# Kernel tuning notes

Hardware: AMD Instinct MI355X
Metric: run time of the kernel (lower is better)

The kernel has to match this reference:

```python
import jax, jax.numpy as jnp
import numpy as np

B, M, D = 512, 100000, 256
EPS = 1e-8  # torch.cosine_similarity eps
TEMP = 10.0  # softmax temperature from source


def setup_inputs() -> dict:
    key = jax.random.key(0)
    kx, kk, kv = jax.random.split(key, 3)
    x = jax.random.normal(kx, (B, D), dtype=jnp.float32)
    memory_keys = jax.random.normal(kk, (M, D), dtype=jnp.float32) * 0.1
    memory_values = jax.random.normal(kv, (M, D), dtype=jnp.float32) * 0.1
    return {"x": x, "memory_keys": memory_keys, "memory_values": memory_values}


def reference(x, memory_keys, memory_values):
    # cosine similarity between x [B,D] and memory_keys [M,D] -> [B,M]
    dots = jnp.einsum("bd,md->bm", x, memory_keys)
    xn = jnp.linalg.norm(x, axis=-1)          # [B]
    kn = jnp.linalg.norm(memory_keys, axis=-1)  # [M]
    denom = jnp.maximum(xn[:, None] * kn[None, :], EPS)
    sims = dots / denom                         # [B,M]
    attn = jax.nn.softmax(sims * TEMP, axis=-1)  # [B,M]
    retrieved = jnp.einsum("bm,md->bd", attn, memory_values)  # [B,D]
    return retrieved, attn
```

## Files before the change

### kernel.cpp

```cpp
#include <hip/hip_runtime.h>
#include <hip/hip_bf16.h>


#define MCOLS 100000
#define MP    100032
#define DDIM  256
#define CHUNK 1664
#define NTFULL 26
#define NCHUNK 61
#define CHUNK1 832
#define NCHUNK1 121
#define NST2  242
#define NSLOT 61
#define ATTN_OFF 131072
#define WS_RXN  0
#define WS_RKN  512
#define WS_RCPL 100512
#define WS_VT_BYTE   1048576ull
#define WS_PART_BYTE 52264960ull
#define WS_KB_BYTE   84246528ull
#define WS_KB_END    (WS_KB_BYTE + 2ull*(size_t)MCOLS*DDIM)

#define GLL(g, l) __builtin_amdgcn_global_load_lds( \
    (const __attribute__((address_space(1))) void*)(g), \
    (__attribute__((address_space(3))) void*)(l), 16, 0, 0)

typedef short short8 __attribute__((ext_vector_type(8)));
typedef float f32x4  __attribute__((ext_vector_type(4)));

static __device__ __forceinline__ unsigned short f2bfu(float f) {
  union { __hip_bfloat16 h; unsigned short u; } cv;
  cv.h = __float2bfloat16(f);
  return cv.u;
}
static __device__ __forceinline__ unsigned int pk2(float a, float b) {
  return (unsigned int)f2bfu(a) | ((unsigned int)f2bfu(b) << 16);
}
static __device__ __forceinline__ short8 pack8(float4 a, float4 b) {
  short8 r;
  r[0] = (short)f2bfu(a.x); r[1] = (short)f2bfu(a.y);
  r[2] = (short)f2bfu(a.z); r[3] = (short)f2bfu(a.w);
  r[4] = (short)f2bfu(b.x); r[5] = (short)f2bfu(b.y);
  r[6] = (short)f2bfu(b.z); r[7] = (short)f2bfu(b.w);
  return r;
}

__global__ void k0_xn(const float* __restrict__ x, float* __restrict__ ws) {
  const int b = blockIdx.x, t = threadIdx.x;
  const float v = x[b*DDIM + t];
  float s = v*v;
  #pragma unroll
  for (int mk = 1; mk <= 32; mk <<= 1) s += __shfl_xor(s, mk);
  __shared__ float ps[4];
  if ((t & 63) == 0) ps[t >> 6] = s;
  __syncthreads();
  if (t == 0) {
    const float tot = ps[0] + ps[1] + ps[2] + ps[3];
    ws[WS_RXN + b] = 10.0f / fmaxf(sqrtf(tot), 1e-12f);
  }
}

template<bool WRITEKB>
__global__ __launch_bounds__(256) void k0c_kn(const float* __restrict__ K,
                                              float* __restrict__ ws) {
  const int t = threadIdx.x;
  const int mg = blockIdx.x*64 + (t >> 2);
  const int qq = t & 3;
  if (mg >= MCOLS) return;
  const float* kp = K + (size_t)mg*DDIM + 64*qq;
  unsigned int* kb = (unsigned int*)((char*)ws + WS_KB_BYTE);
  float ss = 0.f;
  #pragma unroll
  for (int j = 0; j < 8; ++j) {
    const float4 a = *(const float4*)(kp + 8*j);
    const float4 b = *(const float4*)(kp + 8*j + 4);
    ss += a.x*a.x + a.y*a.y + a.z*a.z + a.w*a.w
        + b.x*b.x + b.y*b.y + b.z*b.z + b.w*b.w;
    if (WRITEKB) {
      uint4 u;
      u.x = pk2(a.x, a.y); u.y = pk2(a.z, a.w);
      u.z = pk2(b.x, b.y); u.w = pk2(b.z, b.w);
      const int slot = (8*qq + j) ^ (mg & 7);
      *(uint4*)(kb + (size_t)mg*128 + slot*4) = u;
    }
  }
  ss += __shfl_xor(ss, 1); ss += __shfl_xor(ss, 2);
  if (qq == 0) ws[WS_RKN + mg] = 1.0f / fmaxf(sqrtf(ss), 1e-12f);
}

__global__ __launch_bounds__(256) void k0b_tr(const float* __restrict__ V,
                                              float* __restrict__ ws) {
  const int t = threadIdx.x;
  const int m0 = blockIdx.x * 64;
  __shared__ float vt_f[64][261];
  #pragma unroll
  for (int i = 0; i < 4; ++i) {
    const int ml = (t >> 4) + 16*i;
    const int mg = m0 + ml;
    #pragma unroll
    for (int j = 0; j < 4; ++j) {
      const int d = 4*(t & 15) + 64*j;
      float4 v = make_float4(0.f, 0.f, 0.f, 0.f);
      if (mg < MCOLS) v = *(const float4*)(V + (size_t)mg*DDIM + d);
      vt_f[ml][d] = v.x; vt_f[ml][d+1] = v.y; vt_f[ml][d+2] = v.z; vt_f[ml][d+3] = v.w;
    }
  }
  __syncthreads();
  unsigned short* vt = (unsigned short*)((char*)ws + WS_VT_BYTE);
  const int tl = t & 15;
  const int s = tl >> 1, hf = tl & 1;
  const int mq = 8*s + 4*hf;
  #pragma unroll
  for (int it = 0; it < 16; ++it) {
    const int d = (t >> 4) + 16*it;
    uint2 u;
    u.x = pk2(vt_f[mq+0][d], vt_f[mq+1][d]);
    u.y = pk2(vt_f[mq+2][d], vt_f[mq+3][d]);
    const int sp = s ^ (d & 7);
    *(uint2*)(vt + (size_t)d*MP + m0 + sp*8 + 4*hf) = u;
  }
}

static __device__ __forceinline__ void load_xf(const float* __restrict__ x,
                                               int brow0, int q, int ln,
                                               short8 xf[2][8]) {
  #pragma unroll
  for (int as = 0; as < 2; ++as) {
    const int row = brow0 + 16*as + ln;
    #pragma unroll
    for (int kk = 0; kk < 8; ++kk) {
      const float* p = x + row*DDIM + 32*kk + 8*q;
      xf[as][kk] = pack8(*(const float4*)p, *(const float4*)(p + 4));
    }
  }
}

static __device__ __forceinline__ void stage_k(const char* __restrict__ kb,
                                               int m0, int w, int l,
                                               unsigned short (*klds)[256]) {
  #pragma unroll
  for (int i = 0; i < 4; ++i) {
    int r = m0 + w*8 + i*2 + (l >> 5);
    r = min(r, MCOLS - 1);
    const char* g = kb + (size_t)r*512 + (l & 31)*16;
    char* dst = (char*)&klds[w*8 + i*2][0];
    GLL(g, dst);
  }
}

static __device__ __forceinline__ void stage_vt(const char* __restrict__ vtb,
                                                int m1, int w, int l,
                                                unsigned short (*vtl)[64]) {
  #pragma unroll
  for (int i = 0; i < 4; ++i) {
    const int d = w*32 + i*8 + (l >> 3);
    const int ms = min(m1 + (l & 7)*8, MP - 8);
    const char* g = vtb + ((size_t)d*MP + ms)*2;
    char* dst = (char*)&vtl[w*32 + i*8][0];
    GLL(g, dst);
  }
}

__global__ __launch_bounds__(512, 4) void k1b_sum(const float* __restrict__ x,
                                                  const float* __restrict__ ws,
                                                  float* __restrict__ out) {
  const int bid = blockIdx.x;
  const int c = bid >> 2, rb = bid & 3;
  const int t = threadIdx.x, w = t >> 6, l = t & 63, q = l >> 4, ln = l & 15;
  const int h = w & 1, rg = w >> 1;
  __shared__ __align__(16) unsigned short klds[2][64][256];
  const char* kb = (const char*)ws + WS_KB_BYTE;

  short8 xf[2][8];
  const int brow0 = rb*128 + 32*rg;
  load_xf(x, brow0, q, ln, xf);
  float rxn[2][4];
  #pragma unroll
  for (int as = 0; as < 2; ++as)
    #pragma unroll
    for (int r = 0; r < 4; ++r)
      rxn[as][r] = ws[WS_RXN + brow0 + 16*as + 4*q + r];
  const float* rknw = ws + WS_RKN;
  float lpr[2][4] = {{0.f,0.f,0.f,0.f},{0.f,0.f,0.f,0.f}};
  const int mbase = c*CHUNK1;
  const int nt = min(13, (MCOLS - mbase + 63) >> 6);
  const int l7 = ln & 7;

  stage_k(kb, mbase, w, l, klds[0]);
  __syncthreads();
  for (int mt = 0; mt < nt; ++mt) {
    const int cur = mt & 1;
    const int m0 = mbase + mt*64;
    stage_k(kb, m0 + 64, w, l, klds[cur ^ 1]);
    const char* kbase = (const char*)&klds[cur][0][0];
    const int row0 = 32*h + ln;
    f32x4 acc[2][2];
    #pragma unroll
    for (int as = 0; as < 2; ++as)
      #pragma unroll
      for (int mm = 0; mm < 2; ++mm) { f32x4 z = {0.f,0.f,0.f,0.f}; acc[as][mm] = z; }
    #pragma unroll
    for (int kk = 0; kk < 8; ++kk) {
      const int sl = ((q + 4*kk) ^ l7) << 4;
      const short8 b0 = *(const short8*)(kbase + row0*512 + sl);
      const short8 b1 = *(const short8*)(kbase + (row0 + 16)*512 + sl);
      acc[0][0] = __builtin_amdgcn_mfma_f32_16x16x32_bf16(xf[0][kk], b0, acc[0][0], 0,0,0);
      acc[0][1] = __builtin_amdgcn_mfma_f32_16x16x32_bf16(xf[0][kk], b1, acc[0][1], 0,0,0);
      acc[1][0] = __builtin_amdgcn_mfma_f32_16x16x32_bf16(xf[1][kk], b0, acc[1][0], 0,0,0);
      acc[1][1] = __builtin_amdgcn_mfma_f32_16x16x32_bf16(xf[1][kk], b1, acc[1][1], 0,0,0);
    }
    const int mr0 = m0 + 32*h + ln, mr1 = mr0 + 16;
    const int kr0 = min(mr0, MCOLS-1), kr1 = min(mr1, MCOLS-1);
    const float rk0 = rknw[kr0], rk1 = rknw[kr1];
    const bool ok0 = mr0 < MCOLS, ok1 = mr1 < MCOLS;
    #pragma unroll
    for (int as = 0; as < 2; ++as)
      #pragma unroll
      for (int r = 0; r < 4; ++r)
        lpr[as][r] += (ok0 ? __expf(acc[as][0][r]*rxn[as][r]*rk0) : 0.f)
                    + (ok1 ? __expf(acc[as][1][r]*rxn[as][r]*rk1) : 0.f);
    __syncthreads();
  }
  #pragma unroll
  for (int as = 0; as < 2; ++as)
    #pragma unroll
    for (int r = 0; r < 4; ++r) {
      float s = lpr[as][r];
      s += __shfl_xor(s, 1); s += __shfl_xor(s, 2);
      s += __shfl_xor(s, 4); s += __shfl_xor(s, 8);
      if (ln == 0)
        out[(size_t)(c*2 + h)*512 + brow0 + 16*as + 4*q + r] = s;
    }
}

__global__ void k2_final(const float* __restrict__ out, float* __restrict__ ws) {
  const int b = blockIdx.x, t = threadIdx.x;
  float v = (t < NST2) ? out[(size_t)t*512 + b] : 0.f;
  #pragma unroll
  for (int mk = 1; mk <= 32; mk <<= 1) v += __shfl_xor(v, mk);
  __shared__ float s2[4];
  if ((t & 63) == 0) s2[t >> 6] = v;
  __syncthreads();
  if (t == 0) ws[WS_RCPL + b] = 1.0f / (s2[0] + s2[1] + s2[2] + s2[3]);
}

__global__ __launch_bounds__(512, 2) void k3a_main(const float* __restrict__ x,
                                                   float* __restrict__ ws,
                                                   float* __restrict__ out) {
  const int bid = blockIdx.x;
  const int c = bid >> 2, rb = bid & 3;
  const int t = threadIdx.x, w = t >> 6, l = t & 63, q = l >> 4, ln = l & 15;
  const int h = w & 1, rg = w >> 1;
  __shared__ __align__(16) unsigned short klds[2][64][256];
  __shared__ __align__(16) unsigned short vtl[2][256][64];
  __shared__ __align__(16) unsigned short plds[128][72];
  const char* kb  = (const char*)ws + WS_KB_BYTE;
  const char* vtb = (const char*)ws + WS_VT_BYTE;
  const int R0 = rb*128;

  short8 xf[2][8];
  const int brow0 = R0 + 32*rg;
  load_xf(x, brow0, q, ln, xf);
  float rxn[2][4], rlq[2][4];
  #pragma unroll
  for (int as = 0; as < 2; ++as)
    #pragma unroll
    for (int r = 0; r < 4; ++r) {
      const int row = brow0 + 16*as + 4*q + r;
      rxn[as][r] = ws[WS_RXN  + row];
      rlq[as][r] = ws[WS_RCPL + row];
    }
  f32x4 apv[2][8];
  #pragma unroll
  for (int bs = 0; bs < 2; ++bs)
    #pragma unroll
    for (int dx = 0; dx < 8; ++dx) { f32x4 z = {0.f,0.f,0.f,0.f}; apv[bs][dx] = z; }
  const int b2 = 32*(w & 3), d2 = 128*(w >> 2);
  const float* rknw = ws + WS_RKN;
  float* attn = out + ATTN_OFF;
  const int mbase = c*CHUNK;
  const int nt = min(NTFULL, (MCOLS - mbase + 63) >> 6);
  const int l7 = ln & 7;

  stage_k(kb, mbase, w, l, klds[0]);
  stage_vt(vtb, mbase, w, l, vtl[0]);
  __syncthreads();

  for (int mt = 0; mt < nt; ++mt) {
    const int cur = mt & 1;
    const int m0 = mbase + mt*64;
    stage_k(kb, m0 + 64, w, l, klds[cur ^ 1]);
    const char* kbase = (const char*)&klds[cur][0][0];
    const int row0 = 32*h + ln;
    f32x4 acc[2][2];
    #pragma unroll
    for (int as = 0; as < 2; ++as)
      #pragma unroll
      for (int mm = 0; mm < 2; ++mm) { f32x4 z = {0.f,0.f,0.f,0.f}; acc[as][mm] = z; }
    #pragma unroll
    for (int kk = 0; kk < 8; ++kk) {
      const int sl = ((q + 4*kk) ^ l7) << 4;
      const short8 b0 = *(const short8*)(kbase + row0*512 + sl);
      const short8 b1 = *(const short8*)(kbase + (row0 + 16)*512 + sl);
      acc[0][0] = __builtin_amdgcn_mfma_f32_16x16x32_bf16(xf[0][kk], b0, acc[0][0], 0,0,0);
      acc[0][1] = __builtin_amdgcn_mfma_f32_16x16x32_bf16(xf[0][kk], b1, acc[0][1], 0,0,0);
      acc[1][0] = __builtin_amdgcn_mfma_f32_16x16x32_bf16(xf[1][kk], b0, acc[1][0], 0,0,0);
      acc[1][1] = __builtin_amdgcn_mfma_f32_16x16x32_bf16(xf[1][kk], b1, acc[1][1], 0,0,0);
    }
    const int mr0 = m0 + 32*h + ln, mr1 = mr0 + 16;
    const int kr0 = min(mr0, MCOLS-1), kr1 = min(mr1, MCOLS-1);
    const float rk0 = rknw[kr0], rk1 = rknw[kr1];
    const bool ok0 = mr0 < MCOLS, ok1 = mr1 < MCOLS;
    #pragma unroll
    for (int as = 0; as < 2; ++as)
      #pragma unroll
      for (int r = 0; r < 4; ++r) {
        const int rowl = 32*rg + 16*as + 4*q + r;
        const float p0v = ok0 ? __expf(acc[as][0][r]*rxn[as][r]*rk0) : 0.f;
        const float p1v = ok1 ? __expf(acc[as][1][r]*rxn[as][r]*rk1) : 0.f;
        float* arow = attn + (size_t)(R0 + rowl)*MCOLS;
        if (ok0) arow[mr0] = p0v*rlq[as][r];
        if (ok1) arow[mr1] = p1v*rlq[as][r];
        plds[rowl][32*h + ln]      = f2bfu(p0v);
        plds[rowl][32*h + 16 + ln] = f2bfu(p1v);
      }
    __syncthreads();
    stage_vt(vtb, m0 + 64, w, l, vtl[cur ^ 1]);
    const char* vbase = (const char*)&vtl[cur][0][0];
    const short8 af00 = *(const short8*)&plds[b2 + ln][8*q];
    const short8 af01 = *(const short8*)&plds[b2 + ln][32 + 8*q];
    const short8 af10 = *(const short8*)&plds[b2 + 16 + ln][8*q];
    const short8 af11 = *(const short8*)&plds[b2 + 16 + ln][32 + 8*q];
    const int sl0 = (q ^ l7) << 4, sl1 = ((4 + q) ^ l7) << 4;
    #pragma unroll
    for (int dx = 0; dx < 8; ++dx) {
      const int R = d2 + 16*dx + ln;
      const short8 bv0 = *(const short8*)(vbase + R*128 + sl0);
      const short8 bv1 = *(const short8*)(vbase + R*128 + sl1);
      apv[0][dx] = __builtin_amdgcn_mfma_f32_16x16x32_bf16(af00, bv0, apv[0][dx], 0,0,0);
      apv[0][dx] = __builtin_amdgcn_mfma_f32_16x16x32_bf16(af01, bv1, apv[0][dx], 0,0,0);
      apv[1][dx] = __builtin_amdgcn_mfma_f32_16x16x32_bf16(af10, bv0, apv[1][dx], 0,0,0);
      apv[1][dx] = __builtin_amdgcn_mfma_f32_16x16x32_bf16(af11, bv1, apv[1][dx], 0,0,0);
    }
    __syncthreads();
  }

  float* part = (float*)((char*)ws + WS_PART_BYTE);
  float rlp[2][4];
  #pragma unroll
  for (int bs = 0; bs < 2; ++bs)
    #pragma unroll
    for (int r = 0; r < 4; ++r)
      rlp[bs][r] = ws[WS_RCPL + R0 + b2 + 16*bs + 4*q + r];
  #pragma unroll
  for (int bs = 0; bs < 2; ++bs)
    #pragma unroll
    for (int dx = 0; dx < 8; ++dx)
      #pragma unroll
      for (int r = 0; r < 4; ++r)
        part[((size_t)c*512 + R0 + b2 + 16*bs + 4*q + r)*256 + d2 + 16*dx + ln]
          = apv[bs][dx][r]*rlp[bs][r];
}

__global__ __launch_bounds__(512, 2) void k3b_main(const float* __restrict__ x,
                                                   const float* __restrict__ K,
                                                   float* __restrict__ ws,
                                                   float* __restrict__ out) {
  const int bid = blockIdx.x;
  const int c = bid >> 2, rb = bid & 3;
  const int t = threadIdx.x, w = t >> 6, l = t & 63, q = l >> 4, ln = l & 15;
  const int h = w & 1, rg = w >> 1;
  __shared__ __align__(16) unsigned short plds[2][128][72];
  const int R0 = rb*128;
  short8 xf[2][8];
  const int brow0 = R0 + 32*rg;
  load_xf(x, brow0, q, ln, xf);
  float rxn[2][4];
  #pragma unroll
  for (int as = 0; as < 2; ++as)
    #pragma unroll
    for (int r = 0; r < 4; ++r)
      rxn[as][r] = ws[WS_RXN + brow0 + 16*as + 4*q + r];
  float lpr[2][4] = {{0.f,0.f,0.f,0.f},{0.f,0.f,0.f,0.f}};
  f32x4 apv[2][8];
  #pragma unroll
  for (int bs = 0; bs < 2; ++bs)
    #pragma unroll
    for (int dx = 0; dx < 8; ++dx) { f32x4 z = {0.f,0.f,0.f,0.f}; apv[bs][dx] = z; }
  const int b2 = 32*(w & 3), d2 = 128*(w >> 2);
  const unsigned short* vt = (const unsigned short*)((const char*)ws + WS_VT_BYTE);
  const float* rknw = ws + WS_RKN;
  float* attn = out + ATTN_OFF;
  const int mbase = c*CHUNK;
  const int nt = min(NTFULL, (MCOLS - mbase + 63) >> 6);
  const int l7 = ln & 7;

  for (int mt = 0; mt < nt; ++mt) {
    const int m0 = mbase + mt*64;
    const int mr0 = m0 + 32*h + ln, mr1 = mr0 + 16;
    const int kr0 = min(mr0, MCOLS-1), kr1 = min(mr1, MCOLS-1);
    f32x4 acc[2][2];
    #pragma unroll
    for (int as = 0; as < 2; ++as)
      #pragma unroll
      for (int mm = 0; mm < 2; ++mm) { f32x4 z = {0.f,0.f,0.f,0.f}; acc[as][mm] = z; }
    const float* p0 = K + (size_t)kr0*DDIM + 8*q;
    const float* p1 = K + (size_t)kr1*DDIM + 8*q;
    #pragma unroll
    for (int kk = 0; kk < 8; ++kk) {
      const short8 b0 = pack8(*(const float4*)(p0 + 32*kk), *(const float4*)(p0 + 32*kk + 4));
      const short8 b1 = pack8(*(const float4*)(p1 + 32*kk), *(const float4*)(p1 + 32*kk + 4));
      acc[0][0] = __builtin_amdgcn_mfma_f32_16x16x32_bf16(xf[0][kk], b0, acc[0][0], 0,0,0);
      acc[0][1] = __builtin_amdgcn_mfma_f32_16x16x32_bf16(xf[0][kk], b1, acc[0][1], 0,0,0);
      acc[1][0] = __builtin_amdgcn_mfma_f32_16x16x32_bf16(xf[1][kk], b0, acc[1][0], 0,0,0);
      acc[1][1] = __builtin_amdgcn_mfma_f32_16x16x32_bf16(xf[1][kk], b1, acc[1][1], 0,0,0);
    }
    const float rk0 = rknw[kr0], rk1 = rknw[kr1];
    const bool ok0 = mr0 < MCOLS, ok1 = mr1 < MCOLS;
    #pragma unroll
    for (int as = 0; as < 2; ++as)
      #pragma unroll
      for (int r = 0; r < 4; ++r) {
        const int rowl = 32*rg + 16*as + 4*q + r;
        const float p0v = ok0 ? __expf(acc[as][0][r]*rxn[as][r]*rk0) : 0.f;
        const float p1v = ok1 ? __expf(acc[as][1][r]*rxn[as][r]*rk1) : 0.f;
        float* arow = attn + (size_t)(R0 + rowl)*MCOLS;
        if (ok0) arow[mr0] = p0v;
        if (ok1) arow[mr1] = p1v;
        lpr[as][r] += p0v + p1v;
        plds[mt & 1][rowl][32*h + ln]      = f2bfu(p0v);
        plds[mt & 1][rowl][32*h + 16 + ln] = f2bfu(p1v);
      }
    __syncthreads();
    const unsigned short (*pb)[72] = plds[mt & 1];
    const short8 af00 = *(const short8*)&pb[b2 + ln][8*q];
    const short8 af01 = *(const short8*)&pb[b2 + ln][32 + 8*q];
    const short8 af10 = *(const short8*)&pb[b2 + 16 + ln][8*q];
    const short8 af11 = *(const short8*)&pb[b2 + 16 + ln][32 + 8*q];
    #pragma unroll
    for (int dx = 0; dx < 8; ++dx) {
      const int R = d2 + 16*dx + ln;
      const size_t rbase = (size_t)R*MP + m0;
      const short8 bv0 = *(const short8*)(vt + rbase + ((q     ^ (R & 7)) << 3));
      const short8 bv1 = *(const short8*)(vt + rbase + (((4+q) ^ (R & 7)) << 3));
      apv[0][dx] = __builtin_amdgcn_mfma_f32_16x16x32_bf16(af00, bv0, apv[0][dx], 0,0,0);
      apv[0][dx] = __builtin_amdgcn_mfma_f32_16x16x32_bf16(af01, bv1, apv[0][dx], 0,0,0);
      apv[1][dx] = __builtin_amdgcn_mfma_f32_16x16x32_bf16(af10, bv0, apv[1][dx], 0,0,0);
      apv[1][dx] = __builtin_amdgcn_mfma_f32_16x16x32_bf16(af11, bv1, apv[1][dx], 0,0,0);
    }
  }

  #pragma unroll
  for (int as = 0; as < 2; ++as)
    #pragma unroll
    for (int r = 0; r < 4; ++r) {
      float s = lpr[as][r];
      s += __shfl_xor(s, 1); s += __shfl_xor(s, 2);
      s += __shfl_xor(s, 4); s += __shfl_xor(s, 8);
      if (ln == 0)
        out[(size_t)(c*2 + h)*512 + brow0 + 16*as + 4*q + r] = s;
    }
  float* part = (float*)((char*)ws + WS_PART_BYTE);
  #pragma unroll
  for (int bs = 0; bs < 2; ++bs)
    #pragma unroll
    for (int dx = 0; dx < 8; ++dx)
      #pragma unroll
      for (int r = 0; r < 4; ++r)
        part[((size_t)c*512 + R0 + b2 + 16*bs + 4*q + r)*256 + d2 + 16*dx + ln]
          = apv[bs][dx][r];
}

template<bool NORM>
__global__ void k4_red(const float* __restrict__ ws, float* __restrict__ out) {
  const int b = blockIdx.x, t = threadIdx.x;
  const float* part = (const float*)((const char*)ws + WS_PART_BYTE);
  float acc = 0.f;
  for (int cc = 0; cc < NSLOT; ++cc)
    acc += part[((size_t)cc*512 + b)*256 + t];
  if (!NORM) acc *= ws[WS_RCPL + b];
  out[b*DDIM + t] = acc;
}

__global__ void k5_scale(const float* __restrict__ ws, float* __restrict__ out) {
  const int row = blockIdx.y;
  const int i4 = blockIdx.x*256 + threadIdx.x;
  if (i4 >= MCOLS/4) return;
  const float s = ws[WS_RCPL + row];
  float4* p = (float4*)(out + ATTN_OFF + (size_t)row*MCOLS) + i4;
  float4 v = *p;
  v.x *= s; v.y *= s; v.z *= s; v.w *= s;
  *p = v;
}

extern "C" void kernel_launch(void* const* d_in, const int* in_sizes, int n_in,
                              void* d_out, int out_size, void* d_ws, size_t ws_size,
                              hipStream_t stream) {
  const float* x = (const float*)d_in[0];
  const float* K = (const float*)d_in[1];
  const float* V = (const float*)d_in[2];
  float* out = (float*)d_out;
  float* ws  = (float*)d_ws;
  const bool useKB = ws_size >= WS_KB_END;

  k0_xn<<<512, 256, 0, stream>>>(x, ws);
  if (useKB) k0c_kn<true ><<<1563, 256, 0, stream>>>(K, ws);
  else       k0c_kn<false><<<1563, 256, 0, stream>>>(K, ws);
  k0b_tr<<<MP/64, 256, 0, stream>>>(V, ws);
  if (useKB) {
    k1b_sum<<<484, 512, 0, stream>>>(x, ws, out);
    k2_final<<<512, 256, 0, stream>>>(out, ws);
    k3a_main<<<244, 512, 0, stream>>>(x, ws, out);
    k4_red<true><<<512, 256, 0, stream>>>(ws, out);
  } else {
    k3b_main<<<244, 512, 0, stream>>>(x, K, ws, out);
    k2_final<<<512, 256, 0, stream>>>(out, ws);
    k5_scale<<<dim3((MCOLS/4 + 255)/256, 512), 256, 0, stream>>>(ws, out);
    k4_red<false><<<512, 256, 0, stream>>>(ws, out);
  }
}
```

Baseline: 279.2 us.

## Prenormalize x and keys into bf16, retile softmax kernels to 64-row blocks

After: 250.2 us. 10.4% less time.

```diff
diff --git a/kernel.cpp b/kernel.cpp
--- a/kernel.cpp
+++ b/kernel.cpp
@@ -5,17 +5,16 @@
 #define MCOLS 100000
 #define MP    100032
 #define DDIM  256
-#define CHUNK 1664
-#define NTFULL 26
-#define NCHUNK 61
-#define CHUNK1 832
-#define NCHUNK1 121
-#define NST2  242
-#define NSLOT 61
+#define CHUNK 1792
+#define NTFULL 28
+#define NCHUNK 56
+#define NST2  112
+#define NSLOT 56
 #define ATTN_OFF 131072
 #define WS_RXN  0
 #define WS_RKN  512
 #define WS_RCPL 100512
+#define WS_XB_BYTE   409600ull
 #define WS_VT_BYTE   1048576ull
 #define WS_PART_BYTE 52264960ull
 #define WS_KB_BYTE   84246528ull
@@ -54,10 +53,11 @@
   __shared__ float ps[4];
   if ((t & 63) == 0) ps[t >> 6] = s;
   __syncthreads();
-  if (t == 0) {
-    const float tot = ps[0] + ps[1] + ps[2] + ps[3];
-    ws[WS_RXN + b] = 10.0f / fmaxf(sqrtf(tot), 1e-12f);
-  }
+  const float tot = ps[0] + ps[1] + ps[2] + ps[3];
+  const float r10 = 10.0f / fmaxf(sqrtf(tot), 1e-12f);
+  if (t == 0) ws[WS_RXN + b] = r10;
+  unsigned short* xbp = (unsigned short*)((char*)ws + WS_XB_BYTE);
+  xbp[b*DDIM + t] = f2bfu(v * r10);
 }
 
 template<bool WRITEKB>
@@ -68,24 +68,28 @@
   const int qq = t & 3;
   if (mg >= MCOLS) return;
   const float* kp = K + (size_t)mg*DDIM + 64*qq;
-  unsigned int* kb = (unsigned int*)((char*)ws + WS_KB_BYTE);
+  float4 buf[16];
   float ss = 0.f;
   #pragma unroll
-  for (int j = 0; j < 8; ++j) {
-    const float4 a = *(const float4*)(kp + 8*j);
-    const float4 b = *(const float4*)(kp + 8*j + 4);
-    ss += a.x*a.x + a.y*a.y + a.z*a.z + a.w*a.w
-        + b.x*b.x + b.y*b.y + b.z*b.z + b.w*b.w;
-    if (WRITEKB) {
+  for (int j = 0; j < 16; ++j) {
+    buf[j] = *(const float4*)(kp + 4*j);
+    ss += buf[j].x*buf[j].x + buf[j].y*buf[j].y + buf[j].z*buf[j].z + buf[j].w*buf[j].w;
+  }
+  ss += __shfl_xor(ss, 1); ss += __shfl_xor(ss, 2);
+  const float rk = 1.0f / fmaxf(sqrtf(ss), 1e-12f);
+  if (qq == 0) ws[WS_RKN + mg] = rk;
+  if (WRITEKB) {
+    unsigned int* kb = (unsigned int*)((char*)ws + WS_KB_BYTE);
+    #pragma unroll
+    for (int j = 0; j < 8; ++j) {
+      const float4 a = buf[2*j], b2 = buf[2*j+1];
       uint4 u;
-      u.x = pk2(a.x, a.y); u.y = pk2(a.z, a.w);
-      u.z = pk2(b.x, b.y); u.w = pk2(b.z, b.w);
+      u.x = pk2(a.x*rk, a.y*rk);  u.y = pk2(a.z*rk, a.w*rk);
+      u.z = pk2(b2.x*rk, b2.y*rk); u.w = pk2(b2.z*rk, b2.w*rk);
       const int slot = (8*qq + j) ^ (mg & 7);
       *(uint4*)(kb + (size_t)mg*128 + slot*4) = u;
     }
   }
-  ss += __shfl_xor(ss, 1); ss += __shfl_xor(ss, 2);
-  if (qq == 0) ws[WS_RKN + mg] = 1.0f / fmaxf(sqrtf(ss), 1e-12f);
 }
 
 __global__ __launch_bounds__(256) void k0b_tr(const float* __restrict__ V,
@@ -121,20 +125,6 @@
   }
 }
 
-static __device__ __forceinline__ void load_xf(const float* __restrict__ x,
-                                               int brow0, int q, int ln,
-                                               short8 xf[2][8]) {
-  #pragma unroll
-  for (int as = 0; as < 2; ++as) {
-    const int row = brow0 + 16*as + ln;
-    #pragma unroll
-    for (int kk = 0; kk < 8; ++kk) {
-      const float* p = x + row*DDIM + 32*kk + 8*q;
-      xf[as][kk] = pack8(*(const float4*)p, *(const float4*)(p + 4));
-    }
-  }
-}
-
 static __device__ __forceinline__ void stage_k(const char* __restrict__ kb,
                                                int m0, int w, int l,
                                                unsigned short (*klds)[256]) {
@@ -147,7 +137,6 @@
     GLL(g, dst);
   }
 }
-
 static __device__ __forceinline__ void stage_vt(const char* __restrict__ vtb,
                                                 int m1, int w, int l,
                                                 unsigned short (*vtl)[64]) {
@@ -161,76 +150,62 @@
   }
 }
 
-__global__ __launch_bounds__(512, 4) void k1b_sum(const float* __restrict__ x,
-                                                  const float* __restrict__ ws,
+__global__ __launch_bounds__(512, 4) void k1b_sum(const float* __restrict__ ws,
                                                   float* __restrict__ out) {
   const int bid = blockIdx.x;
-  const int c = bid >> 2, rb = bid & 3;
+  const int xg = bid & 7, i = bid >> 3;
+  const int c = xg + 8*(i % 7), rb = i / 7;
   const int t = threadIdx.x, w = t >> 6, l = t & 63, q = l >> 4, ln = l & 15;
-  const int h = w & 1, rg = w >> 1;
-  __shared__ __align__(16) unsigned short klds[2][64][256];
+  const int ar = w & 3, h = w >> 2, l7 = ln & 7;
+  __shared__ __align__(16) unsigned short klds2[2][64][256];
   const char* kb = (const char*)ws + WS_KB_BYTE;
-
-  short8 xf[2][8];
-  const int brow0 = rb*128 + 32*rg;
-  load_xf(x, brow0, q, ln, xf);
-  float rxn[2][4];
-  #pragma unroll
-  for (int as = 0; as < 2; ++as)
-    #pragma unroll
-    for (int r = 0; r < 4; ++r)
-      rxn[as][r] = ws[WS_RXN + brow0 + 16*as + 4*q + r];
-  const float* rknw = ws + WS_RKN;
-  float lpr[2][4] = {{0.f,0.f,0.f,0.f},{0.f,0.f,0.f,0.f}};
-  const int mbase = c*CHUNK1;
-  const int nt = min(13, (MCOLS - mbase + 63) >> 6);
-  const int l7 = ln & 7;
-
-  stage_k(kb, mbase, w, l, klds[0]);
+  const unsigned short* xb = (const unsigned short*)((const char*)ws + WS_XB_BYTE);
+  const int R0 = rb*64;
+
+  short8 xf[8];
+  {
+    const int row = R0 + 16*ar + ln;
+    #pragma unroll
+    for (int kk = 0; kk < 8; ++kk)
+      xf[kk] = *(const short8*)(xb + row*DDIM + 32*kk + 8*q);
+  }
+  float lpr[4] = {0.f,0.f,0.f,0.f};
+  const int mbase = c*CHUNK;
+  const int nt = min(NTFULL, (MCOLS - mbase + 63) >> 6);
+
+  stage_k(kb, mbase, w, l, klds2[0]);
   __syncthreads();
   for (int mt = 0; mt < nt; ++mt) {
     const int cur = mt & 1;
     const int m0 = mbase + mt*64;
-    stage_k(kb, m0 + 64, w, l, klds[cur ^ 1]);
-    const char* kbase = (const char*)&klds[cur][0][0];
+    if (mt + 1 < nt) stage_k(kb, m0 + 64, w, l, klds2[cur ^ 1]);
+    const char* kbase = (const char*)&klds2[cur][0][0];
     const int row0 = 32*h + ln;
-    f32x4 acc[2][2];
-    #pragma unroll
-    for (int as = 0; as < 2; ++as)
-      #pragma unroll
-      for (int mm = 0; mm < 2; ++mm) { f32x4 z = {0.f,0.f,0.f,0.f}; acc[as][mm] = z; }
+    f32x4 acc[2];
+    { f32x4 z = {0.f,0.f,0.f,0.f}; acc[0] = z; acc[1] = z; }
     #pragma unroll
     for (int kk = 0; kk < 8; ++kk) {
       const int sl = ((q + 4*kk) ^ l7) << 4;
       const short8 b0 = *(const short8*)(kbase + row0*512 + sl);
       const short8 b1 = *(const short8*)(kbase + (row0 + 16)*512 + sl);
-      acc[0][0] = __builtin_amdgcn_mfma_f32_16x16x32_bf16(xf[0][kk], b0, acc[0][0], 0,0,0);
-      acc[0][1] = __builtin_amdgcn_mfma_f32_16x16x32_bf16(xf[0][kk], b1, acc[0][1], 0,0,0);
-      acc[1][0] = __builtin_amdgcn_mfma_f32_16x16x32_bf16(xf[1][kk], b0, acc[1][0], 0,0,0);
-      acc[1][1] = __builtin_amdgcn_mfma_f32_16x16x32_bf16(xf[1][kk], b1, acc[1][1], 0,0,0);
-    }
-    const int mr0 = m0 + 32*h + ln, mr1 = mr0 + 16;
-    const int kr0 = min(mr0, MCOLS-1), kr1 = min(mr1, MCOLS-1);
-    const float rk0 = rknw[kr0], rk1 = rknw[kr1];
+      acc[0] = __builtin_amdgcn_mfma_f32_16x16x32_bf16(xf[kk], b0, acc[0], 0,0,0);
+      acc[1] = __builtin_amdgcn_mfma_f32_16x16x32_bf16(xf[kk], b1, acc[1], 0,0,0);
+    }
+    const int mr0 = m0 + row0, mr1 = mr0 + 16;
     const bool ok0 = mr0 < MCOLS, ok1 = mr1 < MCOLS;
     #pragma unroll
-    for (int as = 0; as < 2; ++as)
-      #pragma unroll
-      for (int r = 0; r < 4; ++r)
-        lpr[as][r] += (ok0 ? __expf(acc[as][0][r]*rxn[as][r]*rk0) : 0.f)
-                    + (ok1 ? __expf(acc[as][1][r]*rxn[as][r]*rk1) : 0.f);
+    for (int r = 0; r < 4; ++r)
+      lpr[r] += (ok0 ? __expf(acc[0][r]) : 0.f) + (ok1 ? __expf(acc[1][r]) : 0.f);
     __syncthreads();
   }
   #pragma unroll
-  for (int as = 0; as < 2; ++as)
-    #pragma unroll
-    for (int r = 0; r < 4; ++r) {
-      float s = lpr[as][r];
-      s += __shfl_xor(s, 1); s += __shfl_xor(s, 2);
-      s += __shfl_xor(s, 4); s += __shfl_xor(s, 8);
-      if (ln == 0)
-        out[(size_t)(c*2 + h)*512 + brow0 + 16*as + 4*q + r] = s;
-    }
+  for (int r = 0; r < 4; ++r) {
+    float s = lpr[r];
+    s += __shfl_xor(s, 1); s += __shfl_xor(s, 2);
+    s += __shfl_xor(s, 4); s += __shfl_xor(s, 8);
+    if (ln == 0)
+      out[(size_t)(c*2 + h)*512 + R0 + 16*ar + 4*q + r] = s;
+  }
 }
 
 __global__ void k2_final(const float* __restrict__ out, float* __restrict__ ws) {
@@ -238,128 +213,116 @@
   float v = (t < NST2) ? out[(size_t)t*512 + b] : 0.f;
   #pragma unroll
   for (int mk = 1; mk <= 32; mk <<= 1) v += __shfl_xor(v, mk);
-  __shared__ float s2[4];
+  __shared__ float s2[2];
   if ((t & 63) == 0) s2[t >> 6] = v;
   __syncthreads();
-  if (t == 0) ws[WS_RCPL + b] = 1.0f / (s2[0] + s2[1] + s2[2] + s2[3]);
-}
-
-__global__ __launch_bounds__(512, 2) void k3a_main(const float* __restrict__ x,
-                                                   float* __restrict__ ws,
+  if (t == 0) ws[WS_RCPL + b] = 1.0f / (s2[0] + s2[1]);
+}
+
+__global__ __launch_bounds__(512, 4) void k3a_main(float* __restrict__ ws,
                                                    float* __restrict__ out) {
   const int bid = blockIdx.x;
-  const int c = bid >> 2, rb = bid & 3;
+  const int xg = bid & 7, i = bid >> 3;
+  const int c = xg + 8*(i % 7), rb = i / 7;
   const int t = threadIdx.x, w = t >> 6, l = t & 63, q = l >> 4, ln = l & 15;
-  const int h = w & 1, rg = w >> 1;
-  __shared__ __align__(16) unsigned short klds[2][64][256];
-  __shared__ __align__(16) unsigned short vtl[2][256][64];
-  __shared__ __align__(16) unsigned short plds[128][72];
+  const int ar = w & 3, h = w >> 2, l7 = ln & 15 & 7;
+  __shared__ __align__(16) unsigned short klds[64][256];
+  __shared__ __align__(16) unsigned short vtl[256][64];
+  __shared__ __align__(16) unsigned short plds[64][64];
   const char* kb  = (const char*)ws + WS_KB_BYTE;
   const char* vtb = (const char*)ws + WS_VT_BYTE;
-  const int R0 = rb*128;
-
-  short8 xf[2][8];
-  const int brow0 = R0 + 32*rg;
-  load_xf(x, brow0, q, ln, xf);
-  float rxn[2][4], rlq[2][4];
-  #pragma unroll
-  for (int as = 0; as < 2; ++as)
-    #pragma unroll
-    for (int r = 0; r < 4; ++r) {
-      const int row = brow0 + 16*as + 4*q + r;
-      rxn[as][r] = ws[WS_RXN  + row];
-      rlq[as][r] = ws[WS_RCPL + row];
-    }
-  f32x4 apv[2][8];
-  #pragma unroll
-  for (int bs = 0; bs < 2; ++bs)
-    #pragma unroll
-    for (int dx = 0; dx < 8; ++dx) { f32x4 z = {0.f,0.f,0.f,0.f}; apv[bs][dx] = z; }
-  const int b2 = 32*(w & 3), d2 = 128*(w >> 2);
-  const float* rknw = ws + WS_RKN;
+  const unsigned short* xb = (const unsigned short*)((const char*)ws + WS_XB_BYTE);
+  const int R0 = rb*64;
+
+  short8 xf[8];
+  {
+    const int row = R0 + 16*ar + ln;
+    #pragma unroll
+    for (int kk = 0; kk < 8; ++kk)
+      xf[kk] = *(const short8*)(xb + row*DDIM + 32*kk + 8*q);
+  }
+  float rlq[4];
+  #pragma unroll
+  for (int r = 0; r < 4; ++r)
+    rlq[r] = ws[WS_RCPL + R0 + 16*ar + 4*q + r];
+  f32x4 apv[8];
+  #pragma unroll
+  for (int dx = 0; dx < 8; ++dx) { f32x4 z = {0.f,0.f,0.f,0.f}; apv[dx] = z; }
+  const int d2 = 128*h;
   float* attn = out + ATTN_OFF;
   const int mbase = c*CHUNK;
   const int nt = min(NTFULL, (MCOLS - mbase + 63) >> 6);
-  const int l7 = ln & 7;
-
-  stage_k(kb, mbase, w, l, klds[0]);
-  stage_vt(vtb, mbase, w, l, vtl[0]);
+  unsigned short* pf = &plds[0][0];
+
+  stage_k(kb, mbase, w, l, klds);
   __syncthreads();
 
   for (int mt = 0; mt < nt; ++mt) {
-    const int cur = mt & 1;
     const int m0 = mbase + mt*64;
-    stage_k(kb, m0 + 64, w, l, klds[cur ^ 1]);
-    const char* kbase = (const char*)&klds[cur][0][0];
+    stage_vt(vtb, m0, w, l, vtl);
     const int row0 = 32*h + ln;
-    f32x4 acc[2][2];
-    #pragma unroll
-    for (int as = 0; as < 2; ++as)
-      #pragma unroll
-      for (int mm = 0; mm < 2; ++mm) { f32x4 z = {0.f,0.f,0.f,0.f}; acc[as][mm] = z; }
+    f32x4 acc[2];
+    { f32x4 z = {0.f,0.f,0.f,0.f}; acc[0] = z; acc[1] = z; }
     #pragma unroll
     for (int kk = 0; kk < 8; ++kk) {
       const int sl = ((q + 4*kk) ^ l7) << 4;
-      const short8 b0 = *(const short8*)(kbase + row0*512 + sl);
-      const short8 b1 = *(const short8*)(kbase + (row0 + 16)*512 + sl);
-      acc[0][0] = __builtin_amdgcn_mfma_f32_16x16x32_bf16(xf[0][kk], b0, acc[0][0], 0,0,0);
-      acc[0][1] = __builtin_amdgcn_mfma_f32_16x16x32_bf16(xf[0][kk], b1, acc[0][1], 0,0,0);
-      acc[1][0] = __builtin_amdgcn_mfma_f32_16x16x32_bf16(xf[1][kk], b0, acc[1][0], 0,0,0);
-      acc[1][1] = __builtin_amdgcn_mfma_f32_16x16x32_bf16(xf[1][kk], b1, acc[1][1], 0,0,0);
-    }
-    const int mr0 = m0 + 32*h + ln, mr1 = mr0 + 16;
-    const int kr0 = min(mr0, MCOLS-1), kr1 = min(mr1, MCOLS-1);
-    const float rk0 = rknw[kr0], rk1 = rknw[kr1];
+      const short8 b0 = *(const short8*)((const char*)&klds[0][0] + row0*512 + sl);
+      const short8 b1 = *(const short8*)((const char*)&klds[0][0] + (row0 + 16)*512 + sl);
+      acc[0] = __builtin_amdgcn_mfma_f32_16x16x32_bf16(xf[kk], b0, acc[0], 0,0,0);
+      acc[1] = __builtin_amdgcn_mfma_f32_16x16x32_bf16(xf[kk], b1, acc[1], 0,0,0);
+    }
+    const int mr0 = m0 + row0, mr1 = mr0 + 16;
     const bool ok0 = mr0 < MCOLS, ok1 = mr1 < MCOLS;
     #pragma unroll
-    for (int as = 0; as < 2; ++as)
-      #pragma unroll
-      for (int r = 0; r < 4; ++r) {
-        const int rowl = 32*rg + 16*as + 4*q + r;
-        const float p0v = ok0 ? __expf(acc[as][0][r]*rxn[as][r]*rk0) : 0.f;
-        const float p1v = ok1 ? __expf(acc[as][1][r]*rxn[as][r]*rk1) : 0.f;
-        float* arow = attn + (size_t)(R0 + rowl)*MCOLS;
-        if (ok0) arow[mr0] = p0v*rlq[as][r];
-        if (ok1) arow[mr1] = p1v*rlq[as][r];
-        plds[rowl][32*h + ln]      = f2bfu(p0v);
-        plds[rowl][32*h + 16 + ln] = f2bfu(p1v);
-      }
+    for (int r = 0; r < 4; ++r) {
+      const int rowl = 16*ar + 4*q + r;
+      const float p0v = ok0 ? __expf(acc[0][r]) : 0.f;
+      const float p1v = ok1 ? __expf(acc[1][r]) : 0.f;
+      float* arow = attn + (size_t)(R0 + rowl)*MCOLS;
+      if (ok0) arow[mr0] = p0v*rlq[r];
+      if (ok1) arow[mr1] = p1v*rlq[r];
+      const int r7 = rowl & 7;
+      pf[rowl*64 + ((((ln>>3) + 4*h    ) ^ r7) << 3) + (ln & 7)] = f2bfu(p0v);
+      pf[rowl*64 + ((((ln>>3) + 4*h + 2) ^ r7) << 3) + (ln & 7)] = f2bfu(p1v);
+    }
     __syncthreads();
-    stage_vt(vtb, m0 + 64, w, l, vtl[cur ^ 1]);
-    const char* vbase = (const char*)&vtl[cur][0][0];
-    const short8 af00 = *(const short8*)&plds[b2 + ln][8*q];
-    const short8 af01 = *(const short8*)&plds[b2 + ln][32 + 8*q];
-    const short8 af10 = *(const short8*)&plds[b2 + 16 + ln][8*q];
-    const short8 af11 = *(const short8*)&plds[b2 + 16 + ln][32 + 8*q];
-    const int sl0 = (q ^ l7) << 4, sl1 = ((4 + q) ^ l7) << 4;
+    if (mt + 1 < nt) stage_k(kb, m0 + 64, w, l, klds);
+    const int prow = 16*ar + ln;
+    const short8 af0 = *(const short8*)(pf + prow*64 + ((q       ^ l7) << 3));
+    const short8 af1 = *(const short8*)(pf + prow*64 + (((4 + q) ^ l7) << 3));
     #pragma unroll
     for (int dx = 0; dx < 8; ++dx) {
       const int R = d2 + 16*dx + ln;
-      const short8 bv0 = *(const short8*)(vbase + R*128 + sl0);
-      const short8 bv1 = *(const short8*)(vbase + R*128 + sl1);
-      apv[0][dx] = __builtin_amdgcn_mfma_f32_16x16x32_bf16(af00, bv0, apv[0][dx], 0,0,0);
-      apv[0][dx] = __builtin_amdgcn_mfma_f32_16x16x32_bf16(af01, bv1, apv[0][dx], 0,0,0);
-      apv[1][dx] = __builtin_amdgcn_mfma_f32_16x16x32_bf16(af10, bv0, apv[1][dx], 0,0,0);
-      apv[1][dx] = __builtin_amdgcn_mfma_f32_16x16x32_bf16(af11, bv1, apv[1][dx], 0,0,0);
+      const char* vr = (const char*)&vtl[0][0] + R*128;
+      const short8 bv0 = *(const short8*)(vr + ((q       ^ l7) << 4));
+      const short8 bv1 = *(const short8*)(vr + (((4 + q) ^ l7) << 4));
+      apv[dx] = __builtin_amdgcn_mfma_f32_16x16x32_bf16(af0, bv0, apv[dx], 0,0,0);
+      apv[dx] = __builtin_amdgcn_mfma_f32_16x16x32_bf16(af1, bv1, apv[dx], 0,0,0);
     }
     __syncthreads();
   }
 
   float* part = (float*)((char*)ws + WS_PART_BYTE);
-  float rlp[2][4];
-  #pragma unroll
-  for (int bs = 0; bs < 2; ++bs)
+  #pragma unroll
+  for (int dx = 0; dx < 8; ++dx)
     #pragma unroll
     for (int r = 0; r < 4; ++r)
-      rlp[bs][r] = ws[WS_RCPL + R0 + b2 + 16*bs + 4*q + r];
-  #pragma unroll
-  for (int bs = 0; bs < 2; ++bs)
-    #pragma unroll
-    for (int dx = 0; dx < 8; ++dx)
-      #pragma unroll
-      for (int r = 0; r < 4; ++r)
-        part[((size_t)c*512 + R0 + b2 + 16*bs + 4*q + r)*256 + d2 + 16*dx + ln]
-          = apv[bs][dx][r]*rlp[bs][r];
+      part[((size_t)c*512 + R0 + 16*ar + 4*q + r)*256 + d2 + 16*dx + ln]
+        = apv[dx][r]*rlq[r];
+}
+
+static __device__ __forceinline__ void load_xf(const float* __restrict__ x,
+                                               int brow0, int q, int ln,
+                                               short8 xf[2][8]) {
+  #pragma unroll
+  for (int as = 0; as < 2; ++as) {
+    const int row = brow0 + 16*as + ln;
+    #pragma unroll
+    for (int kk = 0; kk < 8; ++kk) {
+      const float* p = x + row*DDIM + 32*kk + 8*q;
+      xf[as][kk] = pack8(*(const float4*)p, *(const float4*)(p + 4));
+    }
+  }
 }
 
 __global__ __launch_bounds__(512, 2) void k3b_main(const float* __restrict__ x,
@@ -508,13 +471,13 @@
   else       k0c_kn<false><<<1563, 256, 0, stream>>>(K, ws);
   k0b_tr<<<MP/64, 256, 0, stream>>>(V, ws);
   if (useKB) {
-    k1b_sum<<<484, 512, 0, stream>>>(x, ws, out);
-    k2_final<<<512, 256, 0, stream>>>(out, ws);
-    k3a_main<<<244, 512, 0, stream>>>(x, ws, out);
+    k1b_sum<<<448, 512, 0, stream>>>(ws, out);
+    k2_final<<<512, 128, 0, stream>>>(out, ws);
+    k3a_main<<<448, 512, 0, stream>>>(ws, out);
     k4_red<true><<<512, 256, 0, stream>>>(ws, out);
   } else {
-    k3b_main<<<244, 512, 0, stream>>>(x, K, ws, out);
-    k2_final<<<512, 256, 0, stream>>>(out, ws);
+    k3b_main<<<224, 512, 0, stream>>>(x, K, ws, out);
+    k2_final<<<512, 128, 0, stream>>>(out, ws);
     k5_scale<<<dim3((MCOLS/4 + 255)/256, 512), 256, 0, stream>>>(ws, out);
     k4_red<false><<<512, 256, 0, stream>>>(ws, out);
   }
```
